# Kernel optimization log

Hardware: AMD Instinct MI355X
Metric: run time of the kernel (lower is better)

## Reference

```python
import jax, jax.numpy as jnp
import numpy as np

E = 100    # n_estimators
F = 10     # max_features
D = 100    # input feature dim
N = 8192   # batch
LAT = 2    # latent_dim
ENC_DIMS = [F, F // 2, F // 4, LAT]          # 10 -> 5 -> 2 -> 2
DEC_DIMS = [LAT, D // 4, D // 2, D]          # 2 -> 25 -> 50 -> 100


def _make_mlp(key, dims):
    ws, bs = [], []
    for i, (din, dout) in enumerate(zip(dims[:-1], dims[1:])):
        k = jax.random.fold_in(key, i)
        ws.append(jax.random.normal(k, (E, din, dout), dtype=jnp.float32) * 0.05)
        bs.append(jnp.zeros((E, dout), dtype=jnp.float32))
    return ws, bs


def setup_inputs() -> dict:
    key = jax.random.key(0)
    k_in, k_idx, k_enc, k_hi, k_lo = jax.random.split(key, 5)
    inputs = jax.random.normal(k_in, (N, D), dtype=jnp.float32)
    # per-estimator random feature subsets (original uses choice w/o replacement)
    randsamples = jax.random.randint(k_idx, (E, F), 0, D, dtype=jnp.int32)
    enc_ws, enc_bs = _make_mlp(k_enc, ENC_DIMS)
    hi_ws, hi_bs = _make_mlp(k_hi, DEC_DIMS)
    lo_ws, lo_bs = _make_mlp(k_lo, DEC_DIMS)
    d = {"inputs": inputs, "randsamples": randsamples}
    for i in range(3):
        d[f"enc_w{i}"], d[f"enc_b{i}"] = enc_ws[i], enc_bs[i]
        d[f"hi_w{i}"], d[f"hi_b{i}"] = hi_ws[i], hi_bs[i]
        d[f"lo_w{i}"], d[f"lo_b{i}"] = lo_ws[i], lo_bs[i]
    return d


def _mlp(x, ws, bs):
    # x: [E, N, din]; linear activation throughout (module default)
    for w, b in zip(ws, bs):
        x = jnp.einsum('enf,efg->eng', x, w) + b[:, None, :]
    return x


def reference(inputs, randsamples,
              enc_w0, enc_b0, enc_w1, enc_b1, enc_w2, enc_b2,
              hi_w0, hi_b0, hi_w1, hi_b1, hi_w2, hi_b2,
              lo_w0, lo_b0, lo_w1, lo_b1, lo_w2, lo_b2):
    # batched feature gather: [N, E, F] -> [E, N, F]
    xg = jnp.transpose(jnp.take(inputs, randsamples, axis=1), (1, 0, 2))
    z = _mlp(xg, [enc_w0, enc_w1, enc_w2], [enc_b0, enc_b1, enc_b2])   # [E, N, LAT]
    o_hi = _mlp(z, [hi_w0, hi_w1, hi_w2], [hi_b0, hi_b1, hi_b2])       # [E, N, D]
    o_lo = _mlp(z, [lo_w0, lo_w1, lo_w2], [lo_b0, lo_b1, lo_b2])       # [E, N, D]
    return (o_hi, o_lo)
```

## Files before the change

kernel.cpp:

```cpp
#include <hip/hip_runtime.h>

#define E_  100
#define F_  10
#define D_  100
#define N_  8192
#define TN  256
#define NTILES (N_ / TN)

typedef float f32x4 __attribute__((ext_vector_type(4)));

#define WS_PER_E 624
#define CMB_FLOATS (E_ * WS_PER_E)
#define Z_FLOATS   (2 * E_ * N_)
#define T_FLOATS   (D_ * N_)

template <bool DO_TRANSPOSE>
__global__ __launch_bounds__(128) void prep_kernel(
    const float* __restrict__ inputs,
    const float* __restrict__ enc_w0, const float* __restrict__ enc_b0,
    const float* __restrict__ enc_w1, const float* __restrict__ enc_b1,
    const float* __restrict__ enc_w2, const float* __restrict__ enc_b2,
    const float* __restrict__ hi_w0,  const float* __restrict__ hi_b0,
    const float* __restrict__ hi_w1,  const float* __restrict__ hi_b1,
    const float* __restrict__ hi_w2,  const float* __restrict__ hi_b2,
    const float* __restrict__ lo_w0,  const float* __restrict__ lo_b0,
    const float* __restrict__ lo_w1,  const float* __restrict__ lo_b1,
    const float* __restrict__ lo_w2,  const float* __restrict__ lo_b2,
    float* __restrict__ cmb, float* __restrict__ T)
{
    const int t = threadIdx.x;

    if (DO_TRANSPOSE && blockIdx.x >= E_) {
        const int bi = blockIdx.x - E_;
        const int n0 = (bi >> 2) * 128;
        const int d0 = (bi & 3) * 25;
        const float* rowp = inputs + (size_t)(n0 + t) * D_ + d0;
#pragma unroll 5
        for (int j = 0; j < 25; ++j)
            T[(size_t)(d0 + j) * N_ + n0 + t] = rowp[j];
        return;
    }

    const int e = blockIdx.x;
    float* wsE = cmb + (size_t)e * WS_PER_E;

    {
        const float* w0 = enc_w0 + e * 50;
        const float* w1 = enc_w1 + e * 10;
        const float* w2 = enc_w2 + e * 4;
        const float* b0 = enc_b0 + e * 5;
        const float* b1 = enc_b1 + e * 2;
        const float* b2 = enc_b2 + e * 2;

        __shared__ float sW01[20];
        __shared__ float sB01[2];
        if (t < 20) {
            int f = t >> 1, g = t & 1;
            float s = 0.f;
            for (int k = 0; k < 5; ++k) s += w0[f * 5 + k] * w1[k * 2 + g];
            sW01[t] = s;
        }
        if (t < 2) {
            float s = b1[t];
            for (int k = 0; k < 5; ++k) s += b0[k] * w1[k * 2 + t];
            sB01[t] = s;
        }
        __syncthreads();
        if (t < 20) {
            int f = t >> 1, g2 = t & 1;
            wsE[600 + t] = sW01[f * 2 + 0] * w2[0 * 2 + g2]
                         + sW01[f * 2 + 1] * w2[1 * 2 + g2];
        }
        if (t < 2) {
            wsE[620 + t] = sB01[0] * w2[0 * 2 + t] + sB01[1] * w2[1 * 2 + t] + b2[t];
        }
        __syncthreads();
    }

    __shared__ float sT[100];
    __shared__ float sU[50];
    for (int dec = 0; dec < 2; ++dec) {
        const float* w0 = (dec ? lo_w0 : hi_w0) + e * 50;
        const float* w1 = (dec ? lo_w1 : hi_w1) + e * 1250;
        const float* w2 = (dec ? lo_w2 : hi_w2) + e * 5000;
        const float* b0 = (dec ? lo_b0 : hi_b0) + e * 25;
        const float* b1 = (dec ? lo_b1 : hi_b1) + e * 50;
        const float* b2 = (dec ? lo_b2 : hi_b2) + e * 100;
        float* W = wsE + (dec ? 300 : 0);
        float* B = wsE + (dec ? 500 : 200);

        for (int i = t; i < 100; i += blockDim.x) {
            int a = i / 50, c = i % 50;
            float s = 0.f;
            for (int b = 0; b < 25; ++b) s += w0[a * 25 + b] * w1[b * 50 + c];
            sT[i] = s;
        }
        for (int i = t; i < 50; i += blockDim.x) {
            float s = b1[i];
            for (int b = 0; b < 25; ++b) s += b0[b] * w1[b * 50 + i];
            sU[i] = s;
        }
        __syncthreads();
        for (int i = t; i < 200; i += blockDim.x) {
            int a = i / 100, d = i % 100;
            float s = 0.f;
            for (int c = 0; c < 50; ++c) s += sT[a * 50 + c] * w2[c * 100 + d];
            W[i] = s;
        }
        for (int i = t; i < 100; i += blockDim.x) {
            float s = b2[i];
            for (int c = 0; c < 50; ++c) s += sU[c] * w2[c * 100 + i];
            B[i] = s;
        }
        __syncthreads();
    }
}

__global__ __launch_bounds__(256) void z_kernel(
    const float* __restrict__ cmb, const int* __restrict__ randsamples,
    const float* __restrict__ T, float2* __restrict__ zbuf)
{
    const int e    = blockIdx.x >> 5;
    const int tile = blockIdx.x & (NTILES - 1);
    const int n0   = tile * TN;
    const int t    = threadIdx.x;

    __shared__ float sW[22];
    __shared__ int   sIdx[F_];
    if (t < 22) sW[t] = cmb[(size_t)e * WS_PER_E + 600 + t];
    if (t < F_) sIdx[t] = randsamples[e * F_ + t];
    __syncthreads();

    float z0 = sW[20];
    float z1 = sW[21];
#pragma unroll
    for (int f = 0; f < F_; ++f) {
        const float v = T[(size_t)sIdx[f] * N_ + n0 + t];
        z0 += v * sW[2 * f + 0];
        z1 += v * sW[2 * f + 1];
    }
    zbuf[(size_t)e * N_ + n0 + t] = make_float2(z0, z1);
}

__global__ __launch_bounds__(256) void rancoders_store(
    const float* __restrict__ cmb, const float2* __restrict__ zbuf,
    float* __restrict__ out)
{
    const int b    = blockIdx.x;
    const int half = (b >= E_ * NTILES) ? 1 : 0;
    const int rem  = b - half * E_ * NTILES;
    const int e    = rem >> 5;
    const int tile = rem & (NTILES - 1);
    const int n0   = tile * TN;
    const int t    = threadIdx.x;

    __shared__ __align__(16) float  sW[304];
    __shared__ float2 sZ[TN];

    {
        const float* src = cmb + (size_t)e * WS_PER_E + (half ? 300 : 0);
        for (int i = t; i < 300; i += 256) sW[i] = src[i];
        const float2* zsrc = zbuf + (size_t)e * N_ + n0;
        sZ[t] = zsrc[t];
    }
    __syncthreads();

    const int w    = t >> 6;
    const int l    = t & 63;
    const int h    = l >> 5;
    const int dq   = l & 31;
    const bool act = (dq < 25);
    const int d    = (act ? dq : 24) * 4;

    const f32x4 w0 = *(const f32x4*)&sW[0 + d];
    const f32x4 w1 = *(const f32x4*)&sW[100 + d];
    const f32x4 bb = *(const f32x4*)&sW[200 + d];

    float* dst = out + (size_t)half * E_ * N_ * D_ + (size_t)(e * N_ + n0) * D_;

#pragma unroll 8
    for (int it = 0; it < TN / 16; ++it) {
        const int r0 = it * 16 + w * 4 + h;
        const float2 za = sZ[r0];
        const float2 zb = sZ[r0 + 2];

        f32x4 oa = za.x * w0 + za.y * w1 + bb;
        f32x4 ob = zb.x * w0 + zb.y * w1 + bb;

        if (act) {
            const size_t off = (size_t)r0 * D_ + (size_t)d;
            *(f32x4*)&dst[off]          = oa;
            *(f32x4*)&dst[off + 2 * D_] = ob;
        }
    }
}

template <bool USE_T>
__global__ __launch_bounds__(256) void rancoders_mono(
    const float* __restrict__ inputs, const int* __restrict__ randsamples,
    const float* __restrict__ cmb, const float* __restrict__ T,
    float* __restrict__ out)
{
    const int e    = blockIdx.x >> 5;
    const int tile = blockIdx.x & (NTILES - 1);
    const int n0   = tile * TN;
    const int t    = threadIdx.x;

    __shared__ __align__(16) float sP[WS_PER_E];
    __shared__ int    sIdx[F_];
    __shared__ float2 sZ2[TN];

    const float* wsE = cmb + (size_t)e * WS_PER_E;
    for (int i = t; i < 622; i += 256) sP[i] = wsE[i];
    if (t < F_) sIdx[t] = randsamples[e * F_ + t];
    __syncthreads();

    {
        float z0 = sP[620], z1 = sP[621];
        if (USE_T) {
#pragma unroll
            for (int f = 0; f < F_; ++f) {
                float v = T[(size_t)sIdx[f] * N_ + n0 + t];
                z0 += v * sP[600 + 2 * f + 0];
                z1 += v * sP[600 + 2 * f + 1];
            }
        } else {
            const float* row = inputs + (size_t)(n0 + t) * D_;
#pragma unroll
            for (int f = 0; f < F_; ++f) {
                float v = row[sIdx[f]];
                z0 += v * sP[600 + 2 * f + 0];
                z1 += v * sP[600 + 2 * f + 1];
            }
        }
        sZ2[t] = make_float2(z0, z1);
    }
    __syncthreads();

    const int w    = t >> 6;
    const int l    = t & 63;
    const int h    = l >> 5;
    const int dq   = l & 31;
    const bool act = (dq < 25);
    const int d    = (act ? dq : 24) * 4;

    const f32x4 w0h = *(const f32x4*)&sP[0 + d];
    const f32x4 w1h = *(const f32x4*)&sP[100 + d];
    const f32x4 bh  = *(const f32x4*)&sP[200 + d];
    const f32x4 w0l = *(const f32x4*)&sP[300 + d];
    const f32x4 w1l = *(const f32x4*)&sP[400 + d];
    const f32x4 bl  = *(const f32x4*)&sP[500 + d];

    float* out_hi = out + (size_t)(e * N_ + n0) * D_;
    float* out_lo = out + (size_t)E_ * N_ * D_ + (size_t)(e * N_ + n0) * D_;

#pragma unroll 8
    for (int it = 0; it < TN / 16; ++it) {
        const int r0 = it * 16 + w * 4 + h;
        const float2 za = sZ2[r0];
        const float2 zb = sZ2[r0 + 2];
        f32x4 oha = za.x * w0h + za.y * w1h + bh;
        f32x4 ohb = zb.x * w0h + zb.y * w1h + bh;
        f32x4 ola = za.x * w0l + za.y * w1l + bl;
        f32x4 olb = zb.x * w0l + zb.y * w1l + bl;
        if (act) {
            const size_t off = (size_t)r0 * D_ + (size_t)d;
            *(f32x4*)&out_hi[off]          = oha;
            *(f32x4*)&out_hi[off + 2 * D_] = ohb;
            *(f32x4*)&out_lo[off]          = ola;
            *(f32x4*)&out_lo[off + 2 * D_] = olb;
        }
    }
}

extern "C" void kernel_launch(void* const* d_in, const int* in_sizes, int n_in,
                              void* d_out, int out_size, void* d_ws, size_t ws_size,
                              hipStream_t stream) {
    const float* inputs      = (const float*)d_in[0];
    const int*   randsamples = (const int*)d_in[1];
    const float* enc_w0 = (const float*)d_in[2];
    const float* enc_b0 = (const float*)d_in[3];
    const float* hi_w0  = (const float*)d_in[4];
    const float* hi_b0  = (const float*)d_in[5];
    const float* lo_w0  = (const float*)d_in[6];
    const float* lo_b0  = (const float*)d_in[7];
    const float* enc_w1 = (const float*)d_in[8];
    const float* enc_b1 = (const float*)d_in[9];
    const float* hi_w1  = (const float*)d_in[10];
    const float* hi_b1  = (const float*)d_in[11];
    const float* lo_w1  = (const float*)d_in[12];
    const float* lo_b1  = (const float*)d_in[13];
    const float* enc_w2 = (const float*)d_in[14];
    const float* enc_b2 = (const float*)d_in[15];
    const float* hi_w2  = (const float*)d_in[16];
    const float* hi_b2  = (const float*)d_in[17];
    const float* lo_w2  = (const float*)d_in[18];
    const float* lo_b2  = (const float*)d_in[19];

    float* ws  = (float*)d_ws;
    float* out = (float*)d_out;

    const size_t need_full = (size_t)(CMB_FLOATS + Z_FLOATS + T_FLOATS) * 4;
    const size_t need_t    = (size_t)(CMB_FLOATS + T_FLOATS) * 4;

    float* cmb = ws;

    if (ws_size >= need_full) {
        float*  zbuf = ws + CMB_FLOATS;
        float*  T    = ws + CMB_FLOATS + Z_FLOATS;
        prep_kernel<true><<<E_ + 256, 128, 0, stream>>>(
            inputs, enc_w0, enc_b0, enc_w1, enc_b1, enc_w2, enc_b2,
            hi_w0, hi_b0, hi_w1, hi_b1, hi_w2, hi_b2,
            lo_w0, lo_b0, lo_w1, lo_b1, lo_w2, lo_b2, cmb, T);
        z_kernel<<<E_ * NTILES, 256, 0, stream>>>(
            cmb, randsamples, T, (float2*)zbuf);
        rancoders_store<<<2 * E_ * NTILES, 256, 0, stream>>>(
            cmb, (const float2*)zbuf, out);
    } else if (ws_size >= need_t) {
        float* T = ws + CMB_FLOATS;
        prep_kernel<true><<<E_ + 256, 128, 0, stream>>>(
            inputs, enc_w0, enc_b0, enc_w1, enc_b1, enc_w2, enc_b2,
            hi_w0, hi_b0, hi_w1, hi_b1, hi_w2, hi_b2,
            lo_w0, lo_b0, lo_w1, lo_b1, lo_w2, lo_b2, cmb, T);
        rancoders_mono<true><<<E_ * NTILES, 256, 0, stream>>>(
            inputs, randsamples, cmb, T, out);
    } else {
        prep_kernel<false><<<E_, 128, 0, stream>>>(
            inputs, enc_w0, enc_b0, enc_w1, enc_b1, enc_w2, enc_b2,
            hi_w0, hi_b0, hi_w1, hi_b1, hi_w2, hi_b2,
            lo_w0, lo_b0, lo_w1, lo_b1, lo_w2, lo_b2, cmb, nullptr);
        rancoders_mono<false><<<E_ * NTILES, 256, 0, stream>>>(
            inputs, randsamples, cmb, nullptr, out);
    }
}
```

Measured before the change: 155.3 us.

## Make store kernel persistent with grid-stride over 16-row chunks

The output-store kernel is rewritten as a fixed grid of 2048 blocks that grid-stride over contiguous 1600-float output chunks (16 rows each), instead of one block per estimator-tile that staged weights and latents in LDS. Each chunk now reads its weights and z values straight from global memory (L2-resident) with no shared memory or barrier. The aim is fewer block launches, no sync overhead and a more even, streaming write pattern. In exchange, weights are reloaded from global memory for every chunk, and each iteration issues only a small amount of work per thread.

```diff
diff --git a/kernel.cpp b/kernel.cpp
--- a/kernel.cpp
+++ b/kernel.cpp
@@ -13,6 +13,10 @@
 #define CMB_FLOATS (E_ * WS_PER_E)
 #define Z_FLOATS   (2 * E_ * N_)
 #define T_FLOATS   (D_ * N_)
+
+#define NB_STORE   2048
+#define CHUNK_FL   1600
+#define NCHUNK     (2 * E_ * N_ * D_ / CHUNK_FL)
 
 template <bool DO_TRANSPOSE>
 __global__ __launch_bounds__(128) void prep_kernel(
@@ -146,51 +150,38 @@
     const float* __restrict__ cmb, const float2* __restrict__ zbuf,
     float* __restrict__ out)
 {
-    const int b    = blockIdx.x;
-    const int half = (b >= E_ * NTILES) ? 1 : 0;
-    const int rem  = b - half * E_ * NTILES;
-    const int e    = rem >> 5;
-    const int tile = rem & (NTILES - 1);
-    const int n0   = tile * TN;
-    const int t    = threadIdx.x;
-
-    __shared__ __align__(16) float  sW[304];
-    __shared__ float2 sZ[TN];
-
-    {
-        const float* src = cmb + (size_t)e * WS_PER_E + (half ? 300 : 0);
-        for (int i = t; i < 300; i += 256) sW[i] = src[i];
-        const float2* zsrc = zbuf + (size_t)e * N_ + n0;
-        sZ[t] = zsrc[t];
-    }
-    __syncthreads();
-
-    const int w    = t >> 6;
-    const int l    = t & 63;
-    const int h    = l >> 5;
-    const int dq   = l & 31;
+    const int t  = threadIdx.x;
+    const int w  = t >> 6;
+    const int l  = t & 63;
+    const int h  = l >> 5;
+    const int dq = l & 31;
     const bool act = (dq < 25);
-    const int d    = (act ? dq : 24) * 4;
-
-    const f32x4 w0 = *(const f32x4*)&sW[0 + d];
-    const f32x4 w1 = *(const f32x4*)&sW[100 + d];
-    const f32x4 bb = *(const f32x4*)&sW[200 + d];
-
-    float* dst = out + (size_t)half * E_ * N_ * D_ + (size_t)(e * N_ + n0) * D_;
-
-#pragma unroll 8
-    for (int it = 0; it < TN / 16; ++it) {
-        const int r0 = it * 16 + w * 4 + h;
-        const float2 za = sZ[r0];
-        const float2 zb = sZ[r0 + 2];
+    const int d  = (act ? dq : 24) * 4;
+    const int rr = w * 4 + h;
+
+#pragma unroll 2
+    for (int g = blockIdx.x; g < NCHUNK; g += NB_STORE) {
+        const int eh   = g >> 9;
+        const int half = (eh >= E_) ? 1 : 0;
+        const int e    = eh - half * E_;
+        const int rb   = g & 511;
+        const int n0c  = rb * 16;
+
+        const float* cw = cmb + (size_t)e * WS_PER_E + (half ? 300 : 0);
+        const f32x4 w0 = *(const f32x4*)&cw[d];
+        const f32x4 w1 = *(const f32x4*)&cw[100 + d];
+        const f32x4 bb = *(const f32x4*)&cw[200 + d];
+
+        const float2 za = zbuf[(size_t)e * N_ + n0c + rr];
+        const float2 zb = zbuf[(size_t)e * N_ + n0c + rr + 2];
 
         f32x4 oa = za.x * w0 + za.y * w1 + bb;
         f32x4 ob = zb.x * w0 + zb.y * w1 + bb;
 
         if (act) {
-            const size_t off = (size_t)r0 * D_ + (size_t)d;
-            *(f32x4*)&dst[off]          = oa;
-            *(f32x4*)&dst[off + 2 * D_] = ob;
+            float* dst = out + (size_t)g * CHUNK_FL + (size_t)rr * D_ + d;
+            *(f32x4*)&dst[0]       = oa;
+            *(f32x4*)&dst[2 * D_]  = ob;
         }
     }
 }
@@ -314,7 +305,7 @@
             lo_w0, lo_b0, lo_w1, lo_b1, lo_w2, lo_b2, cmb, T);
         z_kernel<<<E_ * NTILES, 256, 0, stream>>>(
             cmb, randsamples, T, (float2*)zbuf);
-        rancoders_store<<<2 * E_ * NTILES, 256, 0, stream>>>(
+        rancoders_store<<<NB_STORE, 256, 0, stream>>>(
             cmb, (const float2*)zbuf, out);
     } else if (ws_size >= need_t) {
         float* T = ws + CMB_FLOATS;
```

Result: slower. 179.5 us (+15.6%).
